# Optimization experiments

Measured on AMD Instinct MI355X. Metric: run time of the kernel, lower is better.

Reference implementation:

```python
import jax, jax.numpy as jnp
import numpy as np

B, T, N, D, W = 8, 24, 1024, 64, 2
EPS = 1e-5


def setup_inputs() -> dict:
    key = jax.random.key(0)
    ks = jax.random.split(key, 6)
    s = 1.0 / np.sqrt(D)
    x = jax.random.normal(ks[0], (B, T, N, D), dtype=jnp.float32)
    W1 = jax.random.normal(ks[1], (D, D), dtype=jnp.float32) * s
    b1 = jax.random.normal(ks[2], (D,), dtype=jnp.float32) * s
    W2 = jax.random.normal(ks[3], (D, D), dtype=jnp.float32) * s
    b2 = jax.random.normal(ks[4], (D,), dtype=jnp.float32) * s
    gamma = jnp.ones((D,), dtype=jnp.float32)
    beta = jnp.zeros((D,), dtype=jnp.float32)
    # expanded_adj: [N, N*W] = [I | I | ...], then row-normalized (norm_adj ~ D^-1 A)
    adj = jnp.tile(jnp.eye(N, dtype=jnp.float32), (1, W))
    adj = adj / jnp.clip(adj.sum(axis=1, keepdims=True), 1.0, None)
    return {"x": x, "W1": W1, "b1": b1, "W2": W2, "b2": b2,
            "gamma": gamma, "beta": beta, "adj": adj}


def reference(x, W1, b1, W2, b2, gamma, beta, adj):
    Bx, Tx, Nx, Dx = x.shape
    win = adj.shape[1] // Nx
    feat = jnp.pad(x, ((0, 0), (win - 1, 0), (0, 0), (0, 0)))
    g = jnp.stack([feat[:, i:i + Tx] for i in range(win)], axis=2)
    g = g.reshape(Bx, Tx, win * Nx, Dx)
    h1 = jnp.einsum('btmd,ed->btme', g, W1) + b1
    h2 = jnp.einsum('btmd,ed->btme', g, W2) + b2
    a1 = jnp.einsum('nm,btme->btne', adj, h1)  # [B,T,N,D]
    a2 = jnp.einsum('nm,btme->btne', adj, h2)
    full = jax.nn.relu(a1 * a2) + a1
    z = full + x
    mu = z.mean(axis=-1, keepdims=True)
    var = z.var(axis=-1, keepdims=True)
    return (z - mu) * jax.lax.rsqrt(var + EPS) * gamma + beta
```

## Files before the change

### kernel.cpp

```cpp
#include <hip/hip_runtime.h>

#define NN 1024
#define DD 64
#define WW 2
#define MROWS (8 * 24 * 1024)
#define NTILES (MROWS / 16)

typedef float  f32x4  __attribute__((ext_vector_type(4)));
typedef __bf16 bf16x8 __attribute__((ext_vector_type(8)));

__global__ __launch_bounds__(256, 4) void stgcn_kernel(
    const float* __restrict__ x,
    const float* __restrict__ W1,
    const float* __restrict__ b1,
    const float* __restrict__ W2,
    const float* __restrict__ b2,
    const float* __restrict__ gamma,
    const float* __restrict__ beta,
    const float* __restrict__ adj,
    float* __restrict__ out)
{
    __shared__ bf16x8 ldsW[2][8][64];

    const int tid  = threadIdx.x;
    const int lane = tid & 63;
    const int wv   = tid >> 6;
    const int m16  = lane & 15;
    const int quad = lane >> 4;

    for (int s = tid; s < 2 * 8 * 64; s += 256) {
        const int m = s >> 9;
        const int f = (s >> 6) & 7;
        const int l = s & 63;
        const int e = ((f >> 1) << 4) + (l & 15);
        const int d = ((f & 1) << 5) + ((l >> 4) << 3);
        const float* wp = (m ? W2 : W1) + e * DD + d;
        const f32x4 wa = *(const f32x4*)(wp);
        const f32x4 wb = *(const f32x4*)(wp + 4);
        bf16x8 v;
#pragma unroll
        for (int j = 0; j < 4; ++j) {
            v[j]     = (__bf16)wa[j];
            v[j + 4] = (__bf16)wb[j];
        }
        ldsW[m][f][l] = v;
    }
    __syncthreads();

    float b1v[4], b2v[4], gv[4], bev[4];
#pragma unroll
    for (int et = 0; et < 4; ++et) {
        const int e = et * 16 + m16;
        b1v[et] = b1[e];
        b2v[et] = b2[e];
        gv[et]  = gamma[e];
        bev[et] = beta[e];
    }

    const int nWaves = (gridDim.x * blockDim.x) >> 6;
    for (int tile = (blockIdx.x * (blockDim.x >> 6)) + wv; tile < NTILES; tile += nWaves) {
        const int r0 = tile * 16;
        const int t  = (r0 / NN) % 24;
        const int nbase = r0 % NN;

        const int n = nbase + m16;
        const float c0 = adj[n * (NN * WW) + n];
        const float c1 = adj[n * (NN * WW) + NN + n];
        const float cb = c0 + c1;

        const float* xr = x + (r0 + m16) * DD + quad * 8;
        const f32x4 c00 = *(const f32x4*)(xr);
        const f32x4 c01 = *(const f32x4*)(xr + 4);
        const f32x4 c10 = *(const f32x4*)(xr + 32);
        const f32x4 c11 = *(const f32x4*)(xr + 36);
        f32x4 p00 = {0.f,0.f,0.f,0.f}, p01 = {0.f,0.f,0.f,0.f};
        f32x4 p10 = {0.f,0.f,0.f,0.f}, p11 = {0.f,0.f,0.f,0.f};
        if (t > 0) {
            const float* xq = xr - NN * DD;
            p00 = *(const f32x4*)(xq);
            p01 = *(const f32x4*)(xq + 4);
            p10 = *(const f32x4*)(xq + 32);
            p11 = *(const f32x4*)(xq + 36);
        }
        bf16x8 A0, A1;
#pragma unroll
        for (int j = 0; j < 4; ++j) {
            A0[j]     = (__bf16)(c0 * p00[j] + c1 * c00[j]);
            A0[j + 4] = (__bf16)(c0 * p01[j] + c1 * c01[j]);
            A1[j]     = (__bf16)(c0 * p10[j] + c1 * c10[j]);
            A1[j + 4] = (__bf16)(c0 * p11[j] + c1 * c11[j]);
        }

        f32x4 acc1[4], acc2[4];
#pragma unroll
        for (int et = 0; et < 4; ++et) {
            acc1[et] = (f32x4){0.f, 0.f, 0.f, 0.f};
            acc2[et] = (f32x4){0.f, 0.f, 0.f, 0.f};
        }
#pragma unroll
        for (int et = 0; et < 4; ++et) {
            const bf16x8 B10 = ldsW[0][et * 2 + 0][lane];
            const bf16x8 B11 = ldsW[0][et * 2 + 1][lane];
            const bf16x8 B20 = ldsW[1][et * 2 + 0][lane];
            const bf16x8 B21 = ldsW[1][et * 2 + 1][lane];
            acc1[et] = __builtin_amdgcn_mfma_f32_16x16x32_bf16(A0, B10, acc1[et], 0, 0, 0);
            acc1[et] = __builtin_amdgcn_mfma_f32_16x16x32_bf16(A1, B11, acc1[et], 0, 0, 0);
            acc2[et] = __builtin_amdgcn_mfma_f32_16x16x32_bf16(A0, B20, acc2[et], 0, 0, 0);
            acc2[et] = __builtin_amdgcn_mfma_f32_16x16x32_bf16(A1, B21, acc2[et], 0, 0, 0);
        }

        float z[4][4];
        float s[4], s2[4];
#pragma unroll
        for (int reg = 0; reg < 4; ++reg) { s[reg] = 0.f; s2[reg] = 0.f; }

#pragma unroll
        for (int reg = 0; reg < 4; ++reg) {
            const int row = quad * 4 + reg;
            const float cbr = __shfl(cb, row, 64);
#pragma unroll
            for (int et = 0; et < 4; ++et) {
                const int e = et * 16 + m16;
                const float xv = x[(r0 + row) * DD + e];
                const float A1v = acc1[et][reg] + cbr * b1v[et];
                const float A2v = acc2[et][reg] + cbr * b2v[et];
                const float p   = A1v * A2v;
                const float full = (p > 0.f ? p : 0.f) + A1v;
                const float zz = full + xv;
                z[reg][et] = zz;
                s[reg]  += zz;
                s2[reg] += zz * zz;
            }
        }

#pragma unroll
        for (int reg = 0; reg < 4; ++reg) {
            float ss = s[reg], qq = s2[reg];
#pragma unroll
            for (int off = 1; off < 16; off <<= 1) {
                ss += __shfl_xor(ss, off, 64);
                qq += __shfl_xor(qq, off, 64);
            }
            const float mu  = ss * (1.f / 64.f);
            const float var = qq * (1.f / 64.f) - mu * mu;
            const float rs  = rsqrtf(var + 1e-5f);
            const int row = quad * 4 + reg;
#pragma unroll
            for (int et = 0; et < 4; ++et) {
                const int e = et * 16 + m16;
                out[(r0 + row) * DD + e] = (z[reg][et] - mu) * rs * gv[et] + bev[et];
            }
        }
    }
}

extern "C" void kernel_launch(void* const* d_in, const int* in_sizes, int n_in,
                              void* d_out, int out_size, void* d_ws, size_t ws_size,
                              hipStream_t stream) {
    const float* x     = (const float*)d_in[0];
    const float* W1    = (const float*)d_in[1];
    const float* b1    = (const float*)d_in[2];
    const float* W2    = (const float*)d_in[3];
    const float* b2    = (const float*)d_in[4];
    const float* gamma = (const float*)d_in[5];
    const float* beta  = (const float*)d_in[6];
    const float* adj   = (const float*)d_in[7];
    float* out = (float*)d_out;

    dim3 grid(1024), block(256);
    hipLaunchKernelGGL(stgcn_kernel, grid, block, 0, stream,
                       x, W1, b1, W2, b2, gamma, beta, adj, out);
}
```

Before: 133.3 us.

## Chain consecutive time steps per wave to reuse previous-step x loads

Each wave now owns a fixed 16-node slice and walks CHAIN=3 consecutive (b,t) slabs, carrying the current x tile forward as the next step's previous tile. The next slab is prefetched while the current one is processed. This cuts the duplicate reads of the time-shifted input and hoists the adjacency and shuffle setup out of the loop. With 1024 blocks of 4 waves covering 64 node slices × 64 chains it still covers all 192 slabs, but it adds register pressure and fewer waves in flight per unit of work.

```diff
diff --git a/kernel.cpp b/kernel.cpp
--- a/kernel.cpp
+++ b/kernel.cpp
@@ -3,8 +3,9 @@
 #define NN 1024
 #define DD 64
 #define WW 2
-#define MROWS (8 * 24 * 1024)
-#define NTILES (MROWS / 16)
+#define TT 24
+#define NBT 192
+#define CHAIN 3
 
 typedef float  f32x4  __attribute__((ext_vector_type(4)));
 typedef __bf16 bf16x8 __attribute__((ext_vector_type(8)));
@@ -57,38 +58,54 @@
         bev[et] = beta[e];
     }
 
-    const int nWaves = (gridDim.x * blockDim.x) >> 6;
-    for (int tile = (blockIdx.x * (blockDim.x >> 6)) + wv; tile < NTILES; tile += nWaves) {
-        const int r0 = tile * 16;
-        const int t  = (r0 / NN) % 24;
-        const int nbase = r0 % NN;
+    const int waveId = blockIdx.x * 4 + wv;
+    const int nbase  = (waveId & 63) * 16;
+    const int bt0    = (waveId >> 6) * CHAIN;
 
-        const int n = nbase + m16;
-        const float c0 = adj[n * (NN * WW) + n];
-        const float c1 = adj[n * (NN * WW) + NN + n];
-        const float cb = c0 + c1;
+    const int n  = nbase + m16;
+    const float c0 = adj[n * (NN * WW) + n];
+    const float c1 = adj[n * (NN * WW) + NN + n];
+    const float cb = c0 + c1;
+    float cbr[4];
+#pragma unroll
+    for (int reg = 0; reg < 4; ++reg) cbr[reg] = __shfl(cb, quad * 4 + reg, 64);
 
-        const float* xr = x + (r0 + m16) * DD + quad * 8;
-        const f32x4 c00 = *(const f32x4*)(xr);
-        const f32x4 c01 = *(const f32x4*)(xr + 4);
-        const f32x4 c10 = *(const f32x4*)(xr + 32);
-        const f32x4 c11 = *(const f32x4*)(xr + 36);
-        f32x4 p00 = {0.f,0.f,0.f,0.f}, p01 = {0.f,0.f,0.f,0.f};
-        f32x4 p10 = {0.f,0.f,0.f,0.f}, p11 = {0.f,0.f,0.f,0.f};
-        if (t > 0) {
-            const float* xq = xr - NN * DD;
-            p00 = *(const f32x4*)(xq);
-            p01 = *(const f32x4*)(xq + 4);
-            p10 = *(const f32x4*)(xq + 32);
-            p11 = *(const f32x4*)(xq + 36);
+    const float* xr0 = x + ((bt0 * NN + nbase) + m16) * DD + quad * 8;
+    f32x4 cur0 = *(const f32x4*)(xr0);
+    f32x4 cur1 = *(const f32x4*)(xr0 + 4);
+    f32x4 cur2 = *(const f32x4*)(xr0 + 32);
+    f32x4 cur3 = *(const f32x4*)(xr0 + 36);
+    f32x4 prv0 = {0.f,0.f,0.f,0.f}, prv1 = {0.f,0.f,0.f,0.f};
+    f32x4 prv2 = {0.f,0.f,0.f,0.f}, prv3 = {0.f,0.f,0.f,0.f};
+    if ((bt0 % TT) != 0) {
+        const float* xp = xr0 - NN * DD;
+        prv0 = *(const f32x4*)(xp);
+        prv1 = *(const f32x4*)(xp + 4);
+        prv2 = *(const f32x4*)(xp + 32);
+        prv3 = *(const f32x4*)(xp + 36);
+    }
+
+#pragma unroll
+    for (int i = 0; i < CHAIN; ++i) {
+        const int r0 = (bt0 + i) * NN + nbase;
+
+        f32x4 nx0 = {0.f,0.f,0.f,0.f}, nx1 = {0.f,0.f,0.f,0.f};
+        f32x4 nx2 = {0.f,0.f,0.f,0.f}, nx3 = {0.f,0.f,0.f,0.f};
+        if (i + 1 < CHAIN) {
+            const float* xn = x + ((r0 + NN) + m16) * DD + quad * 8;
+            nx0 = *(const f32x4*)(xn);
+            nx1 = *(const f32x4*)(xn + 4);
+            nx2 = *(const f32x4*)(xn + 32);
+            nx3 = *(const f32x4*)(xn + 36);
         }
+
         bf16x8 A0, A1;
 #pragma unroll
         for (int j = 0; j < 4; ++j) {
-            A0[j]     = (__bf16)(c0 * p00[j] + c1 * c00[j]);
-            A0[j + 4] = (__bf16)(c0 * p01[j] + c1 * c01[j]);
-            A1[j]     = (__bf16)(c0 * p10[j] + c1 * c10[j]);
-            A1[j + 4] = (__bf16)(c0 * p11[j] + c1 * c11[j]);
+            A0[j]     = (__bf16)(c0 * prv0[j] + c1 * cur0[j]);
+            A0[j + 4] = (__bf16)(c0 * prv1[j] + c1 * cur1[j]);
+            A1[j]     = (__bf16)(c0 * prv2[j] + c1 * cur2[j]);
+            A1[j + 4] = (__bf16)(c0 * prv3[j] + c1 * cur3[j]);
         }
 
         f32x4 acc1[4], acc2[4];
@@ -117,13 +134,12 @@
 #pragma unroll
         for (int reg = 0; reg < 4; ++reg) {
             const int row = quad * 4 + reg;
-            const float cbr = __shfl(cb, row, 64);
 #pragma unroll
             for (int et = 0; et < 4; ++et) {
                 const int e = et * 16 + m16;
                 const float xv = x[(r0 + row) * DD + e];
-                const float A1v = acc1[et][reg] + cbr * b1v[et];
-                const float A2v = acc2[et][reg] + cbr * b2v[et];
+                const float A1v = acc1[et][reg] + cbr[reg] * b1v[et];
+                const float A2v = acc2[et][reg] + cbr[reg] * b2v[et];
                 const float p   = A1v * A2v;
                 const float full = (p > 0.f ? p : 0.f) + A1v;
                 const float zz = full + xv;
@@ -151,6 +167,9 @@
                 out[(r0 + row) * DD + e] = (z[reg][et] - mu) * rs * gv[et] + bev[et];
             }
         }
+
+        prv0 = cur0; prv1 = cur1; prv2 = cur2; prv3 = cur3;
+        cur0 = nx0;  cur1 = nx1;  cur2 = nx2;  cur3 = nx3;
     }
 }
 
```

Result: slower. 144.6 us (+8.5%).

## Transpose MFMA epilogue through LDS to row-major layout with vectorized stores

Applied to the files above, without the earlier changes.

The MFMA accumulator results are staged through a per-wave padded LDS buffer so each lane reads back contiguous row segments in the same layout as the input load. The residual add then reuses the already-loaded x registers instead of reloading x with scattered scalar loads, and the output is written with 16-byte vector stores instead of strided scalar stores. LayerNorm reduction shrinks to two cross-quad shuffles. The grid is also reduced from 1024 to 768 blocks. This adds LDS traffic and about 17 KB of LDS per block, which may affect occupancy.

```diff
diff --git a/kernel.cpp b/kernel.cpp
--- a/kernel.cpp
+++ b/kernel.cpp
@@ -3,8 +3,10 @@
 #define NN 1024
 #define DD 64
 #define WW 2
+#define TT 24
 #define MROWS (8 * 24 * 1024)
 #define NTILES (MROWS / 16)
+#define ZP 68
 
 typedef float  f32x4  __attribute__((ext_vector_type(4)));
 typedef __bf16 bf16x8 __attribute__((ext_vector_type(8)));
@@ -21,6 +23,7 @@
     float* __restrict__ out)
 {
     __shared__ bf16x8 ldsW[2][8][64];
+    __shared__ float  ldsZ[4][16 * ZP];
 
     const int tid  = threadIdx.x;
     const int lane = tid & 63;
@@ -47,20 +50,28 @@
     }
     __syncthreads();
 
-    float b1v[4], b2v[4], gv[4], bev[4];
+    float b1v[4], b2v[4];
 #pragma unroll
     for (int et = 0; et < 4; ++et) {
         const int e = et * 16 + m16;
         b1v[et] = b1[e];
         b2v[et] = b2[e];
-        gv[et]  = gamma[e];
-        bev[et] = beta[e];
     }
+    f32x4 gLo0 = *(const f32x4*)(gamma + quad * 8);
+    f32x4 gLo1 = *(const f32x4*)(gamma + quad * 8 + 4);
+    f32x4 gHi0 = *(const f32x4*)(gamma + 32 + quad * 8);
+    f32x4 gHi1 = *(const f32x4*)(gamma + 32 + quad * 8 + 4);
+    f32x4 eLo0 = *(const f32x4*)(beta + quad * 8);
+    f32x4 eLo1 = *(const f32x4*)(beta + quad * 8 + 4);
+    f32x4 eHi0 = *(const f32x4*)(beta + 32 + quad * 8);
+    f32x4 eHi1 = *(const f32x4*)(beta + 32 + quad * 8 + 4);
+
+    float* zbuf = &ldsZ[wv][0];
 
     const int nWaves = (gridDim.x * blockDim.x) >> 6;
     for (int tile = (blockIdx.x * (blockDim.x >> 6)) + wv; tile < NTILES; tile += nWaves) {
         const int r0 = tile * 16;
-        const int t  = (r0 / NN) % 24;
+        const int t  = (r0 / NN) % TT;
         const int nbase = r0 % NN;
 
         const int n = nbase + m16;
@@ -69,26 +80,27 @@
         const float cb = c0 + c1;
 
         const float* xr = x + (r0 + m16) * DD + quad * 8;
-        const f32x4 c00 = *(const f32x4*)(xr);
-        const f32x4 c01 = *(const f32x4*)(xr + 4);
-        const f32x4 c10 = *(const f32x4*)(xr + 32);
-        const f32x4 c11 = *(const f32x4*)(xr + 36);
-        f32x4 p00 = {0.f,0.f,0.f,0.f}, p01 = {0.f,0.f,0.f,0.f};
-        f32x4 p10 = {0.f,0.f,0.f,0.f}, p11 = {0.f,0.f,0.f,0.f};
+        const f32x4 cur0 = *(const f32x4*)(xr);
+        const f32x4 cur1 = *(const f32x4*)(xr + 4);
+        const f32x4 cur2 = *(const f32x4*)(xr + 32);
+        const f32x4 cur3 = *(const f32x4*)(xr + 36);
+        f32x4 prv0 = {0.f,0.f,0.f,0.f}, prv1 = {0.f,0.f,0.f,0.f};
+        f32x4 prv2 = {0.f,0.f,0.f,0.f}, prv3 = {0.f,0.f,0.f,0.f};
         if (t > 0) {
             const float* xq = xr - NN * DD;
-            p00 = *(const f32x4*)(xq);
-            p01 = *(const f32x4*)(xq + 4);
-            p10 = *(const f32x4*)(xq + 32);
-            p11 = *(const f32x4*)(xq + 36);
+            prv0 = *(const f32x4*)(xq);
+            prv1 = *(const f32x4*)(xq + 4);
+            prv2 = *(const f32x4*)(xq + 32);
+            prv3 = *(const f32x4*)(xq + 36);
         }
+
         bf16x8 A0, A1;
 #pragma unroll
         for (int j = 0; j < 4; ++j) {
-            A0[j]     = (__bf16)(c0 * p00[j] + c1 * c00[j]);
-            A0[j + 4] = (__bf16)(c0 * p01[j] + c1 * c01[j]);
-            A1[j]     = (__bf16)(c0 * p10[j] + c1 * c10[j]);
-            A1[j + 4] = (__bf16)(c0 * p11[j] + c1 * c11[j]);
+            A0[j]     = (__bf16)(c0 * prv0[j] + c1 * cur0[j]);
+            A0[j + 4] = (__bf16)(c0 * prv1[j] + c1 * cur1[j]);
+            A1[j]     = (__bf16)(c0 * prv2[j] + c1 * cur2[j]);
+            A1[j + 4] = (__bf16)(c0 * prv3[j] + c1 * cur3[j]);
         }
 
         f32x4 acc1[4], acc2[4];
@@ -99,58 +111,58 @@
         }
 #pragma unroll
         for (int et = 0; et < 4; ++et) {
-            const bf16x8 B10 = ldsW[0][et * 2 + 0][lane];
-            const bf16x8 B11 = ldsW[0][et * 2 + 1][lane];
-            const bf16x8 B20 = ldsW[1][et * 2 + 0][lane];
-            const bf16x8 B21 = ldsW[1][et * 2 + 1][lane];
-            acc1[et] = __builtin_amdgcn_mfma_f32_16x16x32_bf16(A0, B10, acc1[et], 0, 0, 0);
-            acc1[et] = __builtin_amdgcn_mfma_f32_16x16x32_bf16(A1, B11, acc1[et], 0, 0, 0);
-            acc2[et] = __builtin_amdgcn_mfma_f32_16x16x32_bf16(A0, B20, acc2[et], 0, 0, 0);
-            acc2[et] = __builtin_amdgcn_mfma_f32_16x16x32_bf16(A1, B21, acc2[et], 0, 0, 0);
+            acc1[et] = __builtin_amdgcn_mfma_f32_16x16x32_bf16(A0, ldsW[0][et*2+0][lane], acc1[et], 0, 0, 0);
+            acc1[et] = __builtin_amdgcn_mfma_f32_16x16x32_bf16(A1, ldsW[0][et*2+1][lane], acc1[et], 0, 0, 0);
+            acc2[et] = __builtin_amdgcn_mfma_f32_16x16x32_bf16(A0, ldsW[1][et*2+0][lane], acc2[et], 0, 0, 0);
+            acc2[et] = __builtin_amdgcn_mfma_f32_16x16x32_bf16(A1, ldsW[1][et*2+1][lane], acc2[et], 0, 0, 0);
         }
 
-        float z[4][4];
-        float s[4], s2[4];
+        float cbr[4];
 #pragma unroll
-        for (int reg = 0; reg < 4; ++reg) { s[reg] = 0.f; s2[reg] = 0.f; }
-
+        for (int reg = 0; reg < 4; ++reg) cbr[reg] = __shfl(cb, quad * 4 + reg, 64);
 #pragma unroll
         for (int reg = 0; reg < 4; ++reg) {
             const int row = quad * 4 + reg;
-            const float cbr = __shfl(cb, row, 64);
 #pragma unroll
             for (int et = 0; et < 4; ++et) {
-                const int e = et * 16 + m16;
-                const float xv = x[(r0 + row) * DD + e];
-                const float A1v = acc1[et][reg] + cbr * b1v[et];
-                const float A2v = acc2[et][reg] + cbr * b2v[et];
+                const float A1v = acc1[et][reg] + cbr[reg] * b1v[et];
+                const float A2v = acc2[et][reg] + cbr[reg] * b2v[et];
                 const float p   = A1v * A2v;
-                const float full = (p > 0.f ? p : 0.f) + A1v;
-                const float zz = full + xv;
-                z[reg][et] = zz;
-                s[reg]  += zz;
-                s2[reg] += zz * zz;
+                zbuf[row * ZP + et * 16 + m16] = (p > 0.f ? p : 0.f) + A1v;
             }
         }
 
+        const float* zr = zbuf + m16 * ZP + quad * 8;
+        f32x4 zLo0 = *(const f32x4*)(zr)      + cur0;
+        f32x4 zLo1 = *(const f32x4*)(zr + 4)  + cur1;
+        f32x4 zHi0 = *(const f32x4*)(zr + 32) + cur2;
+        f32x4 zHi1 = *(const f32x4*)(zr + 36) + cur3;
+
+        float ss = 0.f, qq = 0.f;
 #pragma unroll
-        for (int reg = 0; reg < 4; ++reg) {
-            float ss = s[reg], qq = s2[reg];
+        for (int j = 0; j < 4; ++j) {
+            ss += zLo0[j] + zLo1[j] + zHi0[j] + zHi1[j];
+            qq += zLo0[j]*zLo0[j] + zLo1[j]*zLo1[j] + zHi0[j]*zHi0[j] + zHi1[j]*zHi1[j];
+        }
+        ss += __shfl_xor(ss, 16, 64);  qq += __shfl_xor(qq, 16, 64);
+        ss += __shfl_xor(ss, 32, 64);  qq += __shfl_xor(qq, 32, 64);
+        const float mu  = ss * (1.f / 64.f);
+        const float var = qq * (1.f / 64.f) - mu * mu;
+        const float rs  = rsqrtf(var + 1e-5f);
+
+        float* op = out + (r0 + m16) * DD + quad * 8;
+        f32x4 o0, o1, o2, o3;
 #pragma unroll
-            for (int off = 1; off < 16; off <<= 1) {
-                ss += __shfl_xor(ss, off, 64);
-                qq += __shfl_xor(qq, off, 64);
-            }
-            const float mu  = ss * (1.f / 64.f);
-            const float var = qq * (1.f / 64.f) - mu * mu;
-            const float rs  = rsqrtf(var + 1e-5f);
-            const int row = quad * 4 + reg;
-#pragma unroll
-            for (int et = 0; et < 4; ++et) {
-                const int e = et * 16 + m16;
-                out[(r0 + row) * DD + e] = (z[reg][et] - mu) * rs * gv[et] + bev[et];
-            }
+        for (int j = 0; j < 4; ++j) {
+            o0[j] = (zLo0[j] - mu) * rs * gLo0[j] + eLo0[j];
+            o1[j] = (zLo1[j] - mu) * rs * gLo1[j] + eLo1[j];
+            o2[j] = (zHi0[j] - mu) * rs * gHi0[j] + eHi0[j];
+            o3[j] = (zHi1[j] - mu) * rs * gHi1[j] + eHi1[j];
         }
+        *(f32x4*)(op)      = o0;
+        *(f32x4*)(op + 4)  = o1;
+        *(f32x4*)(op + 32) = o2;
+        *(f32x4*)(op + 36) = o3;
     }
 }
 
@@ -167,7 +179,7 @@
     const float* adj   = (const float*)d_in[7];
     float* out = (float*)d_out;
 
-    dim3 grid(1024), block(256);
+    dim3 grid(768), block(256);
     hipLaunchKernelGGL(stgcn_kernel, grid, block, 0, stream,
                        x, W1, b1, W2, b2, gamma, beta, adj, out);
 }
```

Result: slower. 156.8 us (+17.7%).
